# Performance work log

Hardware: AMD Instinct MI355X
Metric: run time of the kernel (lower is better)

The kernel has to match this reference:

```python
import jax, jax.numpy as jnp
import numpy as np
import math

H_HEAD = 8
D_MODEL = 1024
DEPTH = 12
D_K = D_MODEL // H_HEAD // 2  # 64
LAMBDA_INIT = 0.8 - 0.6 * math.exp(-0.3 * DEPTH)
EPS = 1e-5


def setup_inputs() -> dict:
    key = jax.random.key(0)
    ks = jax.random.split(key, 16)
    B, S, D = 2, 2048, D_MODEL
    std = 1.0 / math.sqrt(D)
    inp = {
        "query": jax.random.normal(ks[0], (B, S, D), jnp.float32),
        "key":   jax.random.normal(ks[1], (B, S, D), jnp.float32),
        "value": jax.random.normal(ks[2], (B, S, D), jnp.float32),
        "wq_w": jax.random.normal(ks[3], (D, D), jnp.float32) * std,
        "wq_b": jnp.zeros((D,), jnp.float32),
        "wk_w": jax.random.normal(ks[4], (D, D), jnp.float32) * std,
        "wk_b": jnp.zeros((D,), jnp.float32),
        "wv_w": jax.random.normal(ks[5], (D, D), jnp.float32) * std,
        "wv_b": jnp.zeros((D,), jnp.float32),
        "fc_w": jax.random.normal(ks[6], (D, D), jnp.float32) * std,
        "fc_b": jnp.zeros((D,), jnp.float32),
        "lambda_q1": jax.random.normal(ks[7], (D_K,), jnp.float32) * 0.1,
        "lambda_k1": jax.random.normal(ks[8], (D_K,), jnp.float32) * 0.1,
        "lambda_q2": jax.random.normal(ks[9], (D_K,), jnp.float32) * 0.1,
        "lambda_k2": jax.random.normal(ks[10], (D_K,), jnp.float32) * 0.1,
        "subln_w": jnp.ones((2 * D_K,), jnp.float32),
    }
    return inp


def _rms_norm(x, w):
    xf = x.astype(jnp.float32)
    out = xf * jax.lax.rsqrt(jnp.mean(xf * xf, axis=-1, keepdims=True) + EPS)
    return out.astype(x.dtype) * w


def reference(query, key, value, wq_w, wq_b, wk_w, wk_b, wv_w, wv_b,
              fc_w, fc_b, lambda_q1, lambda_k1, lambda_q2, lambda_k2, subln_w):
    B, S, D = query.shape
    h, dk = H_HEAD, D_K
    # projections (torch Linear: x @ W^T + b)
    q = (query @ wq_w.T + wq_b).reshape(B, S, 2 * h, dk).transpose(0, 2, 1, 3)   # [B,2h,S,dk]
    k = (key   @ wk_w.T + wk_b).reshape(B, S, 2 * h, dk).transpose(0, 2, 1, 3)   # [B,2h,S,dk]
    v = (value @ wv_w.T + wv_b).reshape(B, S, h, 2 * dk).transpose(0, 2, 1, 3)   # [B,h,S,2dk]

    scores = jnp.einsum('bhqd,bhkd->bhqk', q, k) / math.sqrt(dk)                 # [B,2h,S,S]
    aw = jax.nn.softmax(scores.astype(jnp.float32), axis=-1).astype(scores.dtype)

    lam1 = jnp.exp(jnp.sum(lambda_q1 * lambda_k1).astype(jnp.float32)).astype(q.dtype)
    lam2 = jnp.exp(jnp.sum(lambda_q2 * lambda_k2).astype(jnp.float32)).astype(q.dtype)
    lam = lam1 - lam2 + LAMBDA_INIT

    aw = aw.reshape(B, h, 2, S, S)
    aw = aw[:, :, 0] - lam * aw[:, :, 1]                                          # [B,h,S,S]

    attn = jnp.einsum('bhqk,bhkd->bhqd', aw, v)                                   # [B,h,S,2dk]
    attn = _rms_norm(attn, subln_w) * (1.0 - LAMBDA_INIT)
    attn = attn.transpose(0, 2, 1, 3).reshape(B, S, h * 2 * dk)
    out = attn @ fc_w.T + fc_b
    return (out, aw)
```

## Files before the change

### kernel.cpp

```cpp
#include <hip/hip_runtime.h>
#include <stdint.h>

#define DEV __device__ __forceinline__

typedef short s8v __attribute__((ext_vector_type(8)));
typedef float f4v __attribute__((ext_vector_type(4)));
typedef unsigned short u16;

static constexpr float LAMBDA_INIT = 0.783605766531624464f;
static constexpr float OUT_SCALE   = 0.216394233468375536f;

DEV u16 f2bf(float f) {
    uint32_t u = __builtin_bit_cast(uint32_t, f);
    u += 0x7fffu + ((u >> 16) & 1u);
    return (u16)(u >> 16);
}
DEV float bf2f(u16 v) {
    return __builtin_bit_cast(float, (uint32_t)v << 16);
}

__global__ __launch_bounds__(256)
void cvt_kernel(const float* __restrict__ q, const float* __restrict__ k,
                const float* __restrict__ v, const float* __restrict__ w0,
                const float* __restrict__ w1, const float* __restrict__ w2,
                const float* __restrict__ w3,
                u16* qo, u16* ko, u16* vo, u16* o0, u16* o1, u16* o2, u16* o3)
{
    int bid = blockIdx.x;
    const float* src; u16* dst; int base;
    if      (bid < 2048) { src = q;  dst = qo; base = bid * 2048; }
    else if (bid < 4096) { src = k;  dst = ko; base = (bid - 2048) * 2048; }
    else if (bid < 6144) { src = v;  dst = vo; base = (bid - 4096) * 2048; }
    else if (bid < 6656) { src = w0; dst = o0; base = (bid - 6144) * 2048; }
    else if (bid < 7168) { src = w1; dst = o1; base = (bid - 6656) * 2048; }
    else if (bid < 7680) { src = w2; dst = o2; base = (bid - 7168) * 2048; }
    else                 { src = w3; dst = o3; base = (bid - 7680) * 2048; }
    int i = base + threadIdx.x * 8;
    float4 a = *(const float4*)(src + i);
    float4 b = *(const float4*)(src + i + 4);
    u16 r[8] = { f2bf(a.x), f2bf(a.y), f2bf(a.z), f2bf(a.w),
                 f2bf(b.x), f2bf(b.y), f2bf(b.z), f2bf(b.w) };
    *(s8v*)(dst + i) = *(const s8v*)r;
}

template<int OUT_MODE>
__global__ __launch_bounds__(256)
void gemm128(const u16* __restrict__ A, const u16* __restrict__ W,
             const float* __restrict__ bias, void* __restrict__ Cp)
{
    constexpr int K = 1024;
    __shared__ __align__(16) char smem[OUT_MODE == 2 ? 32768 : 24576];
    const int m0 = blockIdx.x * 128, n0 = blockIdx.y * 64;
    const int t = threadIdx.x, lane = t & 63, wave = t >> 6;
    const int l15 = lane & 15, g = lane >> 4;

    f4v acc[2][4] = {};

    for (int k0 = 0; k0 < K; k0 += 64) {
#pragma unroll
        for (int i = 0; i < 4; ++i) {
            int idx = t + i * 256, row = idx >> 3, piece = idx & 7;
            s8v v = *(const s8v*)(A + (size_t)(m0 + row) * K + k0 + piece * 8);
            *(s8v*)(smem + row * 128 + ((piece * 16) ^ ((row & 7) << 4))) = v;
        }
#pragma unroll
        for (int i = 0; i < 2; ++i) {
            int idx = t + i * 256, row = idx >> 3, piece = idx & 7;
            s8v v = *(const s8v*)(W + (size_t)(n0 + row) * K + k0 + piece * 8);
            *(s8v*)(smem + 16384 + row * 128 + ((piece * 16) ^ ((row & 7) << 4))) = v;
        }
        __syncthreads();
#pragma unroll
        for (int ks = 0; ks < 2; ++ks) {
            s8v af[2], bf4[4];
#pragma unroll
            for (int mt = 0; mt < 2; ++mt) {
                int row = wave * 32 + mt * 16 + l15;
                af[mt] = *(const s8v*)(smem + row * 128 + ((ks * 64 + g * 16) ^ ((l15 & 7) << 4)));
            }
#pragma unroll
            for (int nt = 0; nt < 4; ++nt) {
                int row = nt * 16 + l15;
                bf4[nt] = *(const s8v*)(smem + 16384 + row * 128 + ((ks * 64 + g * 16) ^ ((l15 & 7) << 4)));
            }
#pragma unroll
            for (int mt = 0; mt < 2; ++mt)
#pragma unroll
                for (int nt = 0; nt < 4; ++nt)
                    acc[mt][nt] = __builtin_amdgcn_mfma_f32_16x16x32_bf16(af[mt], bf4[nt], acc[mt][nt], 0, 0, 0);
        }
        __syncthreads();
    }

    float bv[4];
#pragma unroll
    for (int nt = 0; nt < 4; ++nt) bv[nt] = bias[n0 + nt * 16 + l15];

    if (OUT_MODE == 0) {
        u16* rep = (u16*)smem;
#pragma unroll
        for (int mt = 0; mt < 2; ++mt)
#pragma unroll
            for (int nt = 0; nt < 4; ++nt)
#pragma unroll
                for (int r = 0; r < 4; ++r)
                    rep[(wave * 32 + mt * 16 + g * 4 + r) * 64 + nt * 16 + l15] = f2bf(acc[mt][nt][r] + bv[nt]);
        __syncthreads();
        u16* C = (u16*)Cp;
#pragma unroll
        for (int j = 0; j < 4; ++j) {
            int m = j * 32 + (t >> 3), chunk = t & 7;
            s8v v = *(const s8v*)(smem + m * 128 + chunk * 16);
            *(s8v*)(C + (size_t)(m0 + m) * 1024 + n0 + chunk * 8) = v;
        }
    } else if (OUT_MODE == 1) {
        u16* LT = (u16*)smem;
#pragma unroll
        for (int mt = 0; mt < 2; ++mt)
#pragma unroll
            for (int nt = 0; nt < 4; ++nt)
#pragma unroll
                for (int r = 0; r < 4; ++r)
                    LT[(nt * 16 + l15) * 136 + wave * 32 + mt * 16 + g * 4 + r] = f2bf(acc[mt][nt][r] + bv[nt]);
        __syncthreads();
        u16* C = (u16*)Cp;
        const int b = m0 >> 11, s0 = m0 & 2047;
#pragma unroll
        for (int j = 0; j < 4; ++j) {
            int n = j * 16 + (t >> 4), chunk = t & 15;
            s8v v = *(const s8v*)(smem + n * 272 + chunk * 16);
            *(s8v*)(C + ((size_t)b * 1024 + n0 + n) * 2048 + s0 + chunk * 8) = v;
        }
    } else {
        float* rep = (float*)smem;
#pragma unroll
        for (int mt = 0; mt < 2; ++mt)
#pragma unroll
            for (int nt = 0; nt < 4; ++nt)
#pragma unroll
                for (int r = 0; r < 4; ++r)
                    rep[(wave * 32 + mt * 16 + g * 4 + r) * 64 + nt * 16 + l15] = acc[mt][nt][r] + bv[nt];
        __syncthreads();
        float* C = (float*)Cp;
#pragma unroll
        for (int j = 0; j < 8; ++j) {
            int m = j * 16 + (t >> 4), c4 = t & 15;
            float4 v = *(const float4*)(smem + m * 256 + c4 * 16);
            *(float4*)(C + (size_t)(m0 + m) * 1024 + n0 + c4 * 4) = v;
        }
    }
}

__global__ __launch_bounds__(256, 4)
void attn_sum(const u16* __restrict__ Qb, const u16* __restrict__ Kb,
              float* __restrict__ psum)
{
    constexpr int S = 2048, D = 1024;
    __shared__ __align__(16) char smem[16384];
    const int bid0 = blockIdx.x;
    const int bid = (bid0 & 7) * 256 + (bid0 >> 3);
    const int sl = bid & 3, qt = (bid >> 2) & 31, h = (bid >> 7) & 7, b = bid >> 10;
    const int t = threadIdx.x, lane = t & 63, qw = t >> 6;
    const int l15 = lane & 15, g = lane >> 4;
    const int wrow0 = qt * 64 + qw * 16;

    const u16* Qbase = Qb + ((size_t)b * S + wrow0 + l15) * D + h * 128;
    s8v q1[2], q2[2];
#pragma unroll
    for (int ks = 0; ks < 2; ++ks) {
        q1[ks] = *(const s8v*)(Qbase + ks * 32 + g * 8);
        q2[ks] = *(const s8v*)(Qbase + 64 + ks * 32 + g * 8);
    }
    const u16* Ksrc = Kb + (size_t)b * S * D + (size_t)(sl * 512) * D + h * 128;
    const int swz = (l15 & 7) << 4;

    float t1a[4] = {}, t2a[4] = {};
    s8v kreg[4];
#pragma unroll
    for (int i = 0; i < 4; ++i) {
        int idx = t + i * 256, row = idx >> 4, piece = idx & 15;
        kreg[i] = *(const s8v*)(Ksrc + (size_t)row * D + piece * 8);
    }
#pragma unroll
    for (int i = 0; i < 4; ++i) {
        int idx = t + i * 256, row = idx >> 4, piece = idx & 15;
        int sub = piece >> 3, colB = (piece & 7) * 16;
        *(s8v*)(smem + sub * 8192 + row * 128 + (colB ^ ((row & 7) << 4))) = kreg[i];
    }

    for (int kt = 0; kt < 8; ++kt) {
        if (kt < 7) {
            const u16* src = Ksrc + (size_t)(kt + 1) * 64 * D;
#pragma unroll
            for (int i = 0; i < 4; ++i) {
                int idx = t + i * 256, row = idx >> 4, piece = idx & 15;
                kreg[i] = *(const s8v*)(src + (size_t)row * D + piece * 8);
            }
        }
        __syncthreads();
        f4v s1[4] = {}, s2[4] = {};
        __builtin_amdgcn_s_setprio(1);
#pragma unroll
        for (int nt = 0; nt < 4; ++nt)
#pragma unroll
            for (int ks = 0; ks < 2; ++ks) {
                int ro = (nt * 16 + l15) * 128 + ((ks * 64 + g * 16) ^ swz);
                s1[nt] = __builtin_amdgcn_mfma_f32_16x16x32_bf16(q1[ks], *(const s8v*)(smem + ro), s1[nt], 0, 0, 0);
                s2[nt] = __builtin_amdgcn_mfma_f32_16x16x32_bf16(q2[ks], *(const s8v*)(smem + 8192 + ro), s2[nt], 0, 0, 0);
            }
        __builtin_amdgcn_s_setprio(0);
#pragma unroll
        for (int nt = 0; nt < 4; ++nt)
#pragma unroll
            for (int r = 0; r < 4; ++r) {
                t1a[r] += __expf(s1[nt][r] * 0.125f);
                t2a[r] += __expf(s2[nt][r] * 0.125f);
            }
        __syncthreads();
        if (kt < 7) {
#pragma unroll
            for (int i = 0; i < 4; ++i) {
                int idx = t + i * 256, row = idx >> 4, piece = idx & 15;
                int sub = piece >> 3, colB = (piece & 7) * 16;
                *(s8v*)(smem + sub * 8192 + row * 128 + (colB ^ ((row & 7) << 4))) = kreg[i];
            }
        }
    }

#pragma unroll
    for (int r = 0; r < 4; ++r) {
#pragma unroll
        for (int off = 1; off < 16; off <<= 1) {
            t1a[r] += __shfl_xor(t1a[r], off);
            t2a[r] += __shfl_xor(t2a[r], off);
        }
    }
    if (l15 == 0) {
        float* pp = psum + (size_t)(((b * 8 + h) * 2048) + wrow0 + g * 4) * 8;
#pragma unroll
        for (int r = 0; r < 4; ++r) {
            pp[r * 8 + sl]     = t1a[r];
            pp[r * 8 + 4 + sl] = t2a[r];
        }
    }
}

__global__ __launch_bounds__(512, 4)
void attn_kernel(const u16* __restrict__ Qb, const u16* __restrict__ Kb,
                 const u16* __restrict__ Vt, const float* __restrict__ psum,
                 const float* __restrict__ lq1, const float* __restrict__ lk1,
                 const float* __restrict__ lq2, const float* __restrict__ lk2,
                 const float* __restrict__ subw, float* __restrict__ aw,
                 u16* __restrict__ an)
{
    constexpr int S = 2048, D = 1024;
    __shared__ __align__(16) char smem[74752];
    const int bid0 = blockIdx.x;
    const int bid = (bid0 & 7) * 64 + (bid0 >> 3);
    const int qt = bid & 31, h = (bid >> 5) & 7, b = bid >> 8;
    const int t = threadIdx.x, lane = t & 63, w = t >> 6;
    const int qw = w >> 1, kw = w & 1;
    const int l15 = lane & 15, g = lane >> 4;
    const int qrow0 = qt * 64, wrow0 = qrow0 + qw * 16;

    short* P  = (short*)(smem + 65536);
    float* Po = (float*)smem;

    float lam;
    {
        float p1 = lq1[lane] * lk1[lane], p2 = lq2[lane] * lk2[lane];
#pragma unroll
        for (int off = 1; off < 64; off <<= 1) {
            p1 += __shfl_xor(p1, off);
            p2 += __shfl_xor(p2, off);
        }
        lam = expf(p1) - expf(p2) + LAMBDA_INIT;
    }

    const u16* Qbase = Qb + ((size_t)b * S + wrow0 + l15) * D + h * 128;
    s8v q1[2], q2[2];
#pragma unroll
    for (int ks = 0; ks < 2; ++ks) {
        q1[ks] = *(const s8v*)(Qbase + ks * 32 + g * 8);
        q2[ks] = *(const s8v*)(Qbase + 64 + ks * 32 + g * 8);
    }
    const u16* Ksrc = Kb + (size_t)b * S * D + h * 128;
    const u16* Vsrc = Vt + ((size_t)b * 1024 + h * 128) * 2048;
    const int swz = (l15 & 7) << 4;

    float il1[4], il2[4];
    {
        const float* pp = psum + (size_t)(((b * 8 + h) * 2048) + wrow0 + g * 4) * 8;
#pragma unroll
        for (int r = 0; r < 4; ++r) {
            float4 a = *(const float4*)(pp + r * 8);
            float4 c = *(const float4*)(pp + r * 8 + 4);
            il1[r] = 1.f / ((a.x + a.y) + (a.z + a.w));
            il2[r] = 1.f / ((c.x + c.y) + (c.z + c.w));
        }
    }

    s8v kreg[2], vreg[2];
#pragma unroll
    for (int i = 0; i < 2; ++i) {
        int idx = t + i * 512;
        { int row = idx >> 4, piece = idx & 15;
          kreg[i] = *(const s8v*)(Ksrc + (size_t)row * D + piece * 8); }
        { int dd = idx >> 3, piece = idx & 7;
          vreg[i] = *(const s8v*)(Vsrc + (size_t)dd * 2048 + piece * 8); }
    }
#pragma unroll
    for (int i = 0; i < 2; ++i) {
        int idx = t + i * 512;
        { int row = idx >> 4, piece = idx & 15;
          int sub = piece >> 3, colB = (piece & 7) * 16;
          *(s8v*)(smem + sub * 8192 + row * 128 + (colB ^ ((row & 7) << 4))) = kreg[i]; }
        { int dd = idx >> 3, piece = idx & 7;
          *(s8v*)(smem + 16384 + dd * 128 + ((piece * 16) ^ ((dd & 7) << 4))) = vreg[i]; }
    }
#pragma unroll
    for (int i = 0; i < 2; ++i) {
        int idx = t + i * 512;
        { int row = idx >> 4, piece = idx & 15;
          kreg[i] = *(const s8v*)(Ksrc + (size_t)(64 + row) * D + piece * 8); }
        { int dd = idx >> 3, piece = idx & 7;
          vreg[i] = *(const s8v*)(Vsrc + (size_t)dd * 2048 + 64 + piece * 8); }
    }
    __syncthreads();

    f4v po[8] = {};
    float* awb = aw + ((size_t)(b * 8 + h) * S + qrow0) * S;
    const int arow = lane >> 2, acol = kw * 32 + (lane & 3) * 8;

    for (int kt = 0; kt < 32; ++kt) {
        const int kv0 = kt * 64;
        char* cur = smem + (kt & 1) * 32768;
        char* nxt = smem + ((kt + 1) & 1) * 32768;
        if (kt < 31) {
#pragma unroll
            for (int i = 0; i < 2; ++i) {
                int idx = t + i * 512;
                { int row = idx >> 4, piece = idx & 15;
                  int sub = piece >> 3, colB = (piece & 7) * 16;
                  *(s8v*)(nxt + sub * 8192 + row * 128 + (colB ^ ((row & 7) << 4))) = kreg[i]; }
                { int dd = idx >> 3, piece = idx & 7;
                  *(s8v*)(nxt + 16384 + dd * 128 + ((piece * 16) ^ ((dd & 7) << 4))) = vreg[i]; }
            }
        }
        if (kt < 30) {
            const u16* ksp = Ksrc + (size_t)(kv0 + 128) * D;
            const u16* vsp = Vsrc + kv0 + 128;
#pragma unroll
            for (int i = 0; i < 2; ++i) {
                int idx = t + i * 512;
                { int row = idx >> 4, piece = idx & 15;
                  kreg[i] = *(const s8v*)(ksp + (size_t)row * D + piece * 8); }
                { int dd = idx >> 3, piece = idx & 7;
                  vreg[i] = *(const s8v*)(vsp + (size_t)dd * 2048 + piece * 8); }
            }
        }

        f4v s1[2] = {}, s2[2] = {};
        __builtin_amdgcn_s_setprio(1);
#pragma unroll
        for (int nt = 0; nt < 2; ++nt)
#pragma unroll
            for (int ks = 0; ks < 2; ++ks) {
                int ro = (kw * 32 + nt * 16 + l15) * 128 + ((ks * 64 + g * 16) ^ swz);
                s1[nt] = __builtin_amdgcn_mfma_f32_16x16x32_bf16(q1[ks], *(const s8v*)(cur + ro), s1[nt], 0, 0, 0);
                s2[nt] = __builtin_amdgcn_mfma_f32_16x16x32_bf16(q2[ks], *(const s8v*)(cur + 8192 + ro), s2[nt], 0, 0, 0);
            }
        __builtin_amdgcn_s_setprio(0);
#pragma unroll
        for (int nt = 0; nt < 2; ++nt)
#pragma unroll
            for (int r = 0; r < 4; ++r) {
                float p1 = __expf(s1[nt][r] * 0.125f) * il1[r];
                float p2 = __expf(s2[nt][r] * 0.125f) * il2[r];
                P[(qw * 16 + g * 4 + r) * 72 + kw * 32 + nt * 16 + l15] = (short)f2bf(p1 - lam * p2);
            }
        s8v pf = *(const s8v*)(P + (qw * 16 + l15) * 72 + kw * 32 + g * 8);
        __builtin_amdgcn_s_setprio(1);
#pragma unroll
        for (int dn = 0; dn < 8; ++dn) {
            const s8v* vf = (const s8v*)(cur + 16384 + (dn * 16 + l15) * 128 + ((kw * 64 + g * 16) ^ swz));
            po[dn] = __builtin_amdgcn_mfma_f32_16x16x32_bf16(pf, *vf, po[dn], 0, 0, 0);
        }
        __builtin_amdgcn_s_setprio(0);
        {
            s8v a = *(const s8v*)(P + (qw * 16 + arow) * 72 + acol);
            float4 o0 = { bf2f((u16)a[0]), bf2f((u16)a[1]), bf2f((u16)a[2]), bf2f((u16)a[3]) };
            float4 o1 = { bf2f((u16)a[4]), bf2f((u16)a[5]), bf2f((u16)a[6]), bf2f((u16)a[7]) };
            float* dp = awb + (size_t)(qw * 16 + arow) * S + kv0 + acol;
            *(float4*)dp = o0;
            *(float4*)(dp + 4) = o1;
        }
        __syncthreads();
    }

    if (kw == 0) {
#pragma unroll
        for (int dn = 0; dn < 8; ++dn)
#pragma unroll
            for (int r = 0; r < 4; ++r)
                Po[(qw * 16 + g * 4 + r) * 128 + dn * 16 + l15] = po[dn][r];
    }
    __syncthreads();
    if (kw == 1) {
#pragma unroll
        for (int dn = 0; dn < 8; ++dn)
#pragma unroll
            for (int r = 0; r < 4; ++r)
                Po[(qw * 16 + g * 4 + r) * 128 + dn * 16 + l15] += po[dn][r];
    }
    __syncthreads();

    {
        const int row = t >> 3, c0 = (t & 7) * 16;
        float ss = 0.f;
#pragma unroll
        for (int j = 0; j < 4; ++j) {
            float4 v4 = *(const float4*)(Po + row * 128 + c0 + j * 4);
            ss += v4.x * v4.x + v4.y * v4.y + v4.z * v4.z + v4.w * v4.w;
        }
#pragma unroll
        for (int off = 1; off < 8; off <<= 1) ss += __shfl_xor(ss, off);
        float rs = rsqrtf(ss * (1.0f / 128.0f) + 1e-5f) * OUT_SCALE;
        u16* dst = an + ((size_t)b * S + qrow0 + row) * D + h * 128;
#pragma unroll
        for (int j = 0; j < 2; ++j) {
            u16 tmp[8];
#pragma unroll
            for (int e = 0; e < 8; ++e) {
                int c = c0 + j * 8 + e;
                tmp[e] = f2bf(Po[row * 128 + c] * rs * subw[c]);
            }
            *(s8v*)(dst + c0 + j * 8) = *(const s8v*)tmp;
        }
    }
}

extern "C" void kernel_launch(void* const* d_in, const int* in_sizes, int n_in,
                              void* d_out, int out_size, void* d_ws, size_t ws_size,
                              hipStream_t stream)
{
    const float* query = (const float*)d_in[0];
    const float* key   = (const float*)d_in[1];
    const float* value = (const float*)d_in[2];
    const float* wq_w  = (const float*)d_in[3];
    const float* wq_b  = (const float*)d_in[4];
    const float* wk_w  = (const float*)d_in[5];
    const float* wk_b  = (const float*)d_in[6];
    const float* wv_w  = (const float*)d_in[7];
    const float* wv_b  = (const float*)d_in[8];
    const float* fc_w  = (const float*)d_in[9];
    const float* fc_b  = (const float*)d_in[10];
    const float* lq1   = (const float*)d_in[11];
    const float* lk1   = (const float*)d_in[12];
    const float* lq2   = (const float*)d_in[13];
    const float* lk2   = (const float*)d_in[14];
    const float* subw  = (const float*)d_in[15];

    const size_t MB = 1024 * 1024;
    char* ws = (char*)d_ws;
    u16*   Qbf = (u16*)(ws);
    u16*   Kbf = (u16*)(ws + 8 * MB);
    u16*   Vtg = (u16*)(ws + 16 * MB);
    u16*   ANb = (u16*)(ws + 24 * MB);
    u16*   wqb = (u16*)(ws + 32 * MB);
    u16*   wkb = (u16*)(ws + 34 * MB);
    u16*   wvb = (u16*)(ws + 36 * MB);
    u16*   fcb = (u16*)(ws + 38 * MB);
    float* psum = (float*)(ws + 32 * MB);

    float* out0 = (float*)d_out;
    float* awp  = out0 + (size_t)4096 * 1024;
    u16* qx = (u16*)awp;
    u16* kx = qx + (size_t)4096 * 1024;
    u16* vx = kx + (size_t)4096 * 1024;

    cvt_kernel<<<dim3(8192), dim3(256), 0, stream>>>(query, key, value, wq_w, wk_w, wv_w, fc_w,
                                                     qx, kx, vx, wqb, wkb, wvb, fcb);
    dim3 grid(32, 16), blk(256);
    gemm128<0><<<grid, blk, 0, stream>>>(qx, wqb, wq_b, Qbf);
    gemm128<0><<<grid, blk, 0, stream>>>(kx, wkb, wk_b, Kbf);
    gemm128<1><<<grid, blk, 0, stream>>>(vx, wvb, wv_b, Vtg);
    attn_sum<<<dim3(2048), dim3(256), 0, stream>>>(Qbf, Kbf, psum);
    attn_kernel<<<dim3(512), dim3(512), 0, stream>>>(Qbf, Kbf, Vtg, psum, lq1, lk1, lq2, lk2,
                                                     subw, awp, ANb);
    gemm128<2><<<grid, blk, 0, stream>>>(ANb, fcb, fc_b, out0);
}
```

Measured before the change: 196.1 us.

## Double-buffer K tiles in attn_sum and use nontemporal coalesced aw stores

The row-sum kernel now keeps two shared-memory K buffers and prefetches two tiles ahead, which removes one barrier per iteration and overlaps LDS writes with the MFMA work. In the main attention kernel the fp32 attention-weight store is remapped so each lane writes one float4 per half-tile with nontemporal stores, and it is moved ahead of the PV MFMAs. This is meant to reduce write-cache pollution and improve coalescing on the large aw output. The cost is doubled LDS use in attn_sum, which may lower occupancy.

```diff
diff --git a/kernel.cpp b/kernel.cpp
--- a/kernel.cpp
+++ b/kernel.cpp
@@ -4,6 +4,7 @@
 #define DEV __device__ __forceinline__
 
 typedef short s8v __attribute__((ext_vector_type(8)));
+typedef short s4v __attribute__((ext_vector_type(4)));
 typedef float f4v __attribute__((ext_vector_type(4)));
 typedef unsigned short u16;
 
@@ -156,7 +157,7 @@
               float* __restrict__ psum)
 {
     constexpr int S = 2048, D = 1024;
-    __shared__ __align__(16) char smem[16384];
+    __shared__ __align__(16) char smem[32768];
     const int bid0 = blockIdx.x;
     const int bid = (bid0 & 7) * 256 + (bid0 >> 3);
     const int sl = bid & 3, qt = (bid >> 2) & 31, h = (bid >> 7) & 7, b = bid >> 10;
@@ -187,17 +188,32 @@
         int sub = piece >> 3, colB = (piece & 7) * 16;
         *(s8v*)(smem + sub * 8192 + row * 128 + (colB ^ ((row & 7) << 4))) = kreg[i];
     }
+#pragma unroll
+    for (int i = 0; i < 4; ++i) {
+        int idx = t + i * 256, row = idx >> 4, piece = idx & 15;
+        kreg[i] = *(const s8v*)(Ksrc + (size_t)(64 + row) * D + piece * 8);
+    }
+    __syncthreads();
 
     for (int kt = 0; kt < 8; ++kt) {
+        char* cur = smem + (kt & 1) * 16384;
+        char* nxt = smem + ((kt + 1) & 1) * 16384;
         if (kt < 7) {
-            const u16* src = Ksrc + (size_t)(kt + 1) * 64 * D;
+#pragma unroll
+            for (int i = 0; i < 4; ++i) {
+                int idx = t + i * 256, row = idx >> 4, piece = idx & 15;
+                int sub = piece >> 3, colB = (piece & 7) * 16;
+                *(s8v*)(nxt + sub * 8192 + row * 128 + (colB ^ ((row & 7) << 4))) = kreg[i];
+            }
+        }
+        if (kt < 6) {
+            const u16* src = Ksrc + (size_t)(kt + 2) * 64 * D;
 #pragma unroll
             for (int i = 0; i < 4; ++i) {
                 int idx = t + i * 256, row = idx >> 4, piece = idx & 15;
                 kreg[i] = *(const s8v*)(src + (size_t)row * D + piece * 8);
             }
         }
-        __syncthreads();
         f4v s1[4] = {}, s2[4] = {};
         __builtin_amdgcn_s_setprio(1);
 #pragma unroll
@@ -205,8 +221,8 @@
 #pragma unroll
             for (int ks = 0; ks < 2; ++ks) {
                 int ro = (nt * 16 + l15) * 128 + ((ks * 64 + g * 16) ^ swz);
-                s1[nt] = __builtin_amdgcn_mfma_f32_16x16x32_bf16(q1[ks], *(const s8v*)(smem + ro), s1[nt], 0, 0, 0);
-                s2[nt] = __builtin_amdgcn_mfma_f32_16x16x32_bf16(q2[ks], *(const s8v*)(smem + 8192 + ro), s2[nt], 0, 0, 0);
+                s1[nt] = __builtin_amdgcn_mfma_f32_16x16x32_bf16(q1[ks], *(const s8v*)(cur + ro), s1[nt], 0, 0, 0);
+                s2[nt] = __builtin_amdgcn_mfma_f32_16x16x32_bf16(q2[ks], *(const s8v*)(cur + 8192 + ro), s2[nt], 0, 0, 0);
             }
         __builtin_amdgcn_s_setprio(0);
 #pragma unroll
@@ -217,14 +233,6 @@
                 t2a[r] += __expf(s2[nt][r] * 0.125f);
             }
         __syncthreads();
-        if (kt < 7) {
-#pragma unroll
-            for (int i = 0; i < 4; ++i) {
-                int idx = t + i * 256, row = idx >> 4, piece = idx & 15;
-                int sub = piece >> 3, colB = (piece & 7) * 16;
-                *(s8v*)(smem + sub * 8192 + row * 128 + (colB ^ ((row & 7) << 4))) = kreg[i];
-            }
-        }
     }
 
 #pragma unroll
@@ -330,7 +338,8 @@
 
     f4v po[8] = {};
     float* awb = aw + ((size_t)(b * 8 + h) * S + qrow0) * S;
-    const int arow = lane >> 2, acol = kw * 32 + (lane & 3) * 8;
+    const int drl = lane >> 3;
+    const int dc4 = (lane & 7) * 4;
 
     for (int kt = 0; kt < 32; ++kt) {
         const int kv0 = kt * 64;
@@ -379,6 +388,15 @@
                 float p2 = __expf(s2[nt][r] * 0.125f) * il2[r];
                 P[(qw * 16 + g * 4 + r) * 72 + kw * 32 + nt * 16 + l15] = (short)f2bf(p1 - lam * p2);
             }
+
+#pragma unroll
+        for (int half = 0; half < 2; ++half) {
+            int row = qw * 16 + half * 8 + drl;
+            s4v pv = *(const s4v*)(P + row * 72 + kw * 32 + dc4);
+            f4v o = { bf2f((u16)pv.x), bf2f((u16)pv.y), bf2f((u16)pv.z), bf2f((u16)pv.w) };
+            __builtin_nontemporal_store(o, (f4v*)(awb + (size_t)row * S + kv0 + kw * 32 + dc4));
+        }
+
         s8v pf = *(const s8v*)(P + (qw * 16 + l15) * 72 + kw * 32 + g * 8);
         __builtin_amdgcn_s_setprio(1);
 #pragma unroll
@@ -387,14 +405,6 @@
             po[dn] = __builtin_amdgcn_mfma_f32_16x16x32_bf16(pf, *vf, po[dn], 0, 0, 0);
         }
         __builtin_amdgcn_s_setprio(0);
-        {
-            s8v a = *(const s8v*)(P + (qw * 16 + arow) * 72 + acol);
-            float4 o0 = { bf2f((u16)a[0]), bf2f((u16)a[1]), bf2f((u16)a[2]), bf2f((u16)a[3]) };
-            float4 o1 = { bf2f((u16)a[4]), bf2f((u16)a[5]), bf2f((u16)a[6]), bf2f((u16)a[7]) };
-            float* dp = awb + (size_t)(qw * 16 + arow) * S + kv0 + acol;
-            *(float4*)dp = o0;
-            *(float4*)(dp + 4) = o1;
-        }
         __syncthreads();
     }
 
```

After: 190.4 us, median of 2. 1.03x faster.
